# Performance work log

Measured on AMD Instinct MI355X. Metric: run time of the kernel, lower is better.

Reference implementation:

```python
import jax, jax.numpy as jnp
import numpy as np

N = 50000      # nodes in the block
M = 10         # mailbox_size
H = 8          # attention heads
DIN = 128      # dim_in (per-mail message dim)
DOUT = 128     # dim_out (memory dim)
DT = 128       # dim_time
LN_EPS = 1e-5
LRELU_SLOPE = 0.2


def setup_inputs() -> dict:
    key = jax.random.key(0)
    ks = jax.random.split(key, 16)
    s = 0.05  # small init scale for weights
    return {
        # forward tensor args
        "mem": jax.random.normal(ks[0], (N, DOUT), jnp.float32),
        "mem_input": jax.random.normal(ks[1], (N, M * DIN), jnp.float32),
        "ts": jax.random.uniform(ks[2], (N,), jnp.float32) * 100.0,
        "mail_ts": jax.random.uniform(ks[3], (N, M), jnp.float32) * 100.0,
        # learned parameters (torch Linear convention: W is [out, in])
        "wq_w": jax.random.normal(ks[4], (DOUT, DOUT), jnp.float32) * s,
        "wq_b": jnp.zeros((DOUT,), jnp.float32),
        "wk_w": jax.random.normal(ks[5], (DOUT, DIN + DT), jnp.float32) * s,
        "wk_b": jnp.zeros((DOUT,), jnp.float32),
        "wv_w": jax.random.normal(ks[6], (DOUT, DIN + DT), jnp.float32) * s,
        "wv_b": jnp.zeros((DOUT,), jnp.float32),
        "ln_g": jnp.ones((DOUT,), jnp.float32),
        "ln_b": jnp.zeros((DOUT,), jnp.float32),
        "mlp_w": jax.random.normal(ks[7], (DOUT, DOUT), jnp.float32) * s,
        "mlp_b": jnp.zeros((DOUT,), jnp.float32),
        # TimeEncode: cos(dt * te_w + te_b), te_w = 1/10^linspace(0,9,DT) as in TGN
        "te_w": (1.0 / (10.0 ** np.linspace(0, 9, DT))).astype(np.float32),
        "te_b": jnp.zeros((DT,), jnp.float32),
    }


def reference(mem, mem_input, ts, mail_ts,
              wq_w, wq_b, wk_w, wk_b, wv_w, wv_b,
              ln_g, ln_b, mlp_w, mlp_b, te_w, te_b):
    n = mem.shape[0]
    # Q: [n, H, Dh]
    Q = (mem @ wq_w.T + wq_b).reshape(n, H, -1)
    # mails: [n, M, DIN]
    mails = mem_input.reshape(n, M, -1)
    # time encoding of (src ts - mail ts): [n, M, DT]
    dt = ts[:, None] - mail_ts
    time_feat = jnp.cos(dt[:, :, None] * te_w + te_b)
    mails = jnp.concatenate([mails, time_feat], axis=2)  # [n, M, DIN+DT]
    K = (mails @ wk_w.T + wk_b).reshape(n, M, H, -1)
    V = (mails @ wv_w.T + wv_b).reshape(n, M, H, -1)
    # elementwise QK reduction over head dim, LeakyReLU, softmax over mailbox
    att = jnp.einsum('nhd,nmhd->nmh', Q, K)
    att = jax.nn.leaky_relu(att, LRELU_SLOPE)
    att = jax.nn.softmax(att, axis=1)          # (att_dropout = identity in eval)
    rst = jnp.einsum('nmh,nmhd->nhd', att, V).reshape(n, -1)
    rst = rst + mem                             # residual
    # LayerNorm
    mu = rst.mean(axis=-1, keepdims=True)
    var = ((rst - mu) ** 2).mean(axis=-1, keepdims=True)
    rst = (rst - mu) / jnp.sqrt(var + LN_EPS) * ln_g + ln_b
    # MLP + (dropout = identity in eval) + ReLU
    rst = rst @ mlp_w.T + mlp_b
    return jax.nn.relu(rst)
```

## Files before the change

### kernel.cpp

```cpp
#include <hip/hip_runtime.h>
#include <hip/hip_bf16.h>

#define N_NODES 50000
#define NB 32
#define NTILES 1563
#define PGRID 512
#define LN_EPS 1e-5f
#define SLOPE 0.2f

typedef __attribute__((ext_vector_type(8))) short bf16x8;
typedef __attribute__((ext_vector_type(4))) float f32x4;

__device__ __forceinline__ int imin(int a, int b){ return a < b ? a : b; }

__device__ __forceinline__ short f2bf(float f){
  union { float f; unsigned u; } v; v.f = f;
  unsigned r = v.u + 0x7fffu + ((v.u >> 16) & 1u);
  return (short)(r >> 16);
}

__device__ __forceinline__ float rsum16_dpp(float x){
  asm volatile(
    "s_nop 1\n\t"
    "v_add_f32_dpp %0, %0, %0 row_ror:8 row_mask:0xf bank_mask:0xf\n\t"
    "s_nop 1\n\t"
    "v_add_f32_dpp %0, %0, %0 row_ror:4 row_mask:0xf bank_mask:0xf\n\t"
    "s_nop 1\n\t"
    "v_add_f32_dpp %0, %0, %0 row_ror:2 row_mask:0xf bank_mask:0xf\n\t"
    "s_nop 1\n\t"
    "v_add_f32_dpp %0, %0, %0 row_ror:1 row_mask:0xf bank_mask:0xf"
    : "+v"(x));
  return x;
}

__device__ __forceinline__ unsigned cvtpk(float a, float b){
  unsigned r;
  asm("v_cvt_pk_bf16_f32 %0, %1, %2" : "=v"(r) : "v"(a), "v"(b));
  return r;
}

__device__ __forceinline__ bf16x8 pack8(float4 a, float4 b){
  union { unsigned u[4]; bf16x8 v; } r;
  r.u[0] = cvtpk(a.x, a.y); r.u[1] = cvtpk(a.z, a.w);
  r.u[2] = cvtpk(b.x, b.y); r.u[3] = cvtpk(b.z, b.w);
  return r.v;
}

#define WKP 0
#define WVP 32768
#define WQP 65536
#define MLPP 81920

__global__ __launch_bounds__(256) void prep_pack(
    const float* __restrict__ wq, const float* __restrict__ wk,
    const float* __restrict__ wv, const float* __restrict__ mlp,
    unsigned short* __restrict__ wsP)
{
  int idx = blockIdx.x * 256 + threadIdx.x;
  const float* src; int base, K, local;
  if (idx < 32768)      { src = wk;  base = WKP;  local = idx;         K = 256; }
  else if (idx < 65536) { src = wv;  base = WVP;  local = idx - 32768; K = 256; }
  else if (idx < 81920) { src = wq;  base = WQP;  local = idx - 65536; K = 128; }
  else if (idx < 98304) { src = mlp; base = MLPP; local = idx - 81920; K = 128; }
  else return;
  int i  = local & 7;
  int l  = (local >> 3) & 63;
  int nt = (local >> 9) & 7;
  int ks = local >> 12;
  int row = nt * 16 + (l & 15);
  int k   = ks * 32 + ((l >> 4) << 3) + i;
  wsP[base + local] = (unsigned short)f2bf(src[row * K + k]);
}

__device__ __forceinline__ void stage_write(
    unsigned short* sAp, const float* sTs, const float* sMts,
    const float* sTeW, const float* sTeB,
    float4 f0, float4 f1, int srow, int skc, int ssw, int sg, int m)
{
  float dt = sTs[srow] - sMts[srow*10 + m];
  const float4* tw = (const float4*)(sTeW + skc);
  const float4* tb = (const float4*)(sTeB + skc);
  float4 w0 = tw[0], w1 = tw[1];
  float4 b0 = tb[0], b1 = tb[1];
  float4 c0, c1;
  c0.x=__cosf(dt*w0.x+b0.x); c0.y=__cosf(dt*w0.y+b0.y); c0.z=__cosf(dt*w0.z+b0.z); c0.w=__cosf(dt*w0.w+b0.w);
  c1.x=__cosf(dt*w1.x+b1.x); c1.y=__cosf(dt*w1.y+b1.y); c1.z=__cosf(dt*w1.z+b1.z); c1.w=__cosf(dt*w1.w+b1.w);
  bf16x8* dst = (bf16x8*)sAp;
  dst[srow*32 + (sg ^ ssw)]      = pack8(f0, f1);
  dst[srow*32 + 16 + (sg ^ ssw)] = pack8(c0, c1);
}

__global__ __launch_bounds__(512, 2) void fused_tmu(
    const float* __restrict__ mem, const float* __restrict__ mem_input,
    const float* __restrict__ ts, const float* __restrict__ mail_ts,
    const float* __restrict__ wq_b, const float* __restrict__ wk_b,
    const float* __restrict__ wv_b, const float* __restrict__ ln_g,
    const float* __restrict__ ln_b, const float* __restrict__ mlp_b,
    const float* __restrict__ te_w, const float* __restrict__ te_b,
    const unsigned short* __restrict__ wsP, float* __restrict__ out)
{
  __shared__ __align__(16) unsigned short sA[2 * NB * 256];
  __shared__ float sTs[NB];
  __shared__ float sMts[NB * 10];
  __shared__ float sTeW[128], sTeB[128];
  __shared__ float sRed[NB * 16];

  const int tid  = threadIdx.x;
  const int lane = tid & 63;
  const int wid  = tid >> 6;
  const int l15  = lane & 15;
  const int lg   = lane >> 4;

  const int srow = tid >> 4;
  const int sg   = tid & 15;
  const int skc  = sg << 3;
  const int ssw  = srow & 7;

  if (tid < 128){ sTeW[tid] = te_w[tid]; sTeB[tid] = te_b[tid]; }

  const int c = wid * 16 + l15;
  float qb = wq_b[c], kb = wk_b[c], vb = wv_b[c];
  float lgv = ln_g[c], lbv = ln_b[c], mbv = mlp_b[c];

  const bf16x8* wsv = (const bf16x8*)wsP;
  bf16x8 wkf[8], wvf[8];
  #pragma unroll
  for (int ks = 0; ks < 8; ks++){
    wkf[ks] = wsv[WKP/8 + (ks*8 + wid)*64 + lane];
    wvf[ks] = wsv[WVP/8 + (ks*8 + wid)*64 + lane];
  }

  f32x4 z4 = {0.f, 0.f, 0.f, 0.f};

  for (int tb = blockIdx.x; tb < NTILES; tb += PGRID){
    const int node0 = tb * NB;
    const int sgn = imin(node0 + srow, N_NODES - 1);
    const float* miBase = mem_input + (size_t)sgn * 1280 + skc;

    float4 fm0, fm1, fa0, fa1;
    {
      const float4* mp = (const float4*)(mem + (size_t)sgn * 128 + skc);
      fm0 = mp[0]; fm1 = mp[1];
      const float4* mi0 = (const float4*)(miBase);
      fa0 = mi0[0]; fa1 = mi0[1];
    }
    if (tid < NB) sTs[tid] = ts[imin(node0 + tid, N_NODES - 1)];
    if (tid < NB * 10){
      int nn = tid / 10, mm = tid - nn * 10;
      sMts[tid] = mail_ts[(size_t)imin(node0 + nn, N_NODES - 1) * 10 + mm];
    }
    {
      bf16x8* dst = (bf16x8*)sA;
      dst[NB*32 + srow*32 + (sg ^ ssw)] = pack8(fm0, fm1);
    }
    bf16x8 wqf[4];
    #pragma unroll
    for (int ks = 0; ks < 4; ks++)
      wqf[ks] = wsv[WQP/8 + (ks*8 + wid)*64 + lane];

    __syncthreads();

    stage_write(sA, sTs, sMts, sTeW, sTeB, fa0, fa1, srow, skc, ssw, sg, 0);
    { const float4* mi1 = (const float4*)(miBase + 128); fa0 = mi1[0]; fa1 = mi1[1]; }

    f32x4 qac[2];
    qac[0] = (f32x4){qb, qb, qb, qb};
    qac[1] = qac[0];
    {
      const bf16x8* P1 = (const bf16x8*)sA + NB*32;
      #pragma unroll
      for (int ntr = 0; ntr < 2; ntr++){
        int r = ntr*16 + l15, rs = r & 7;
        #pragma unroll
        for (int ks = 0; ks < 4; ks++){
          bf16x8 af = P1[r*32 + ((ks*4 + lg) ^ rs)];
          qac[ntr] = __builtin_amdgcn_mfma_f32_16x16x32_bf16(af, wqf[ks], qac[ntr], 0, 0, 0);
        }
      }
    }

    __syncthreads();

    f32x4 pv[2] = {z4, z4};
    f32x4 sm[2] = {z4, z4};
    for (int m = 0; m < 10; m++){
      const bf16x8* P = (const bf16x8*)sA + (m & 1) * NB*32;
      #pragma unroll
      for (int ntr = 0; ntr < 2; ntr++){
        int r = ntr*16 + l15, rs = r & 7;
        f32x4 ka = z4, va = z4;
        #pragma unroll
        for (int ks = 0; ks < 8; ks++){
          bf16x8 af = P[r*32 + ((ks*4 + lg) ^ rs)];
          ka = __builtin_amdgcn_mfma_f32_16x16x32_bf16(af, wkf[ks], ka, 0, 0, 0);
          va = __builtin_amdgcn_mfma_f32_16x16x32_bf16(af, wvf[ks], va, 0, 0, 0);
        }
        #pragma unroll
        for (int j = 0; j < 4; j++){
          float lv = (ka[j] + kb) * qac[ntr][j];
          lv = rsum16_dpp(lv);
          lv = fmaxf(lv, SLOPE * lv);
          lv = fminf(lv, 60.f);
          float p = __expf(lv);
          sm[ntr][j] += p;
          pv[ntr][j] += p * va[j];
        }
      }
      if (m < 9){
        stage_write(sA + ((m+1) & 1) * NB*256, sTs, sMts, sTeW, sTeB,
                    fa0, fa1, srow, skc, ssw, sg, m+1);
        if (m < 8){
          const float4* mi = (const float4*)(miBase + (size_t)(m+2)*128);
          fa0 = mi[0]; fa1 = mi[1];
        }
      }
      __syncthreads();
    }

    float rstv[2][4];
    #pragma unroll
    for (int ntr = 0; ntr < 2; ntr++)
      #pragma unroll
      for (int j = 0; j < 4; j++){
        int gn = imin(node0 + ntr*16 + lg*4 + j, N_NODES - 1);
        rstv[ntr][j] = pv[ntr][j] / sm[ntr][j] + vb + mem[(size_t)gn * 128 + c];
      }
    #pragma unroll
    for (int ntr = 0; ntr < 2; ntr++)
      #pragma unroll
      for (int j = 0; j < 4; j++){
        float s = rsum16_dpp(rstv[ntr][j]);
        float q = rsum16_dpp(rstv[ntr][j] * rstv[ntr][j]);
        if (l15 == 0){
          int nl = ntr*16 + lg*4 + j;
          sRed[nl*16 + wid*2    ] = s;
          sRed[nl*16 + wid*2 + 1] = q;
        }
      }
    __syncthreads();
    #pragma unroll
    for (int ntr = 0; ntr < 2; ntr++)
      #pragma unroll
      for (int j = 0; j < 4; j++){
        int nl = ntr*16 + lg*4 + j;
        float sum = 0.f, sq = 0.f;
        #pragma unroll
        for (int w = 0; w < 8; w++){
          sum += sRed[nl*16 + w*2];
          sq  += sRed[nl*16 + w*2 + 1];
        }
        float mu  = sum * (1.f/128.f);
        float var = sq * (1.f/128.f) - mu*mu;
        float rs  = rsqrtf(var + LN_EPS);
        float y = (rstv[ntr][j] - mu) * rs * lgv + lbv;
        sA[nl*256 + ((c >> 3) ^ (nl & 7))*8 + (c & 7)] = (unsigned short)f2bf(y);
      }

    bf16x8 mlpf[4];
    #pragma unroll
    for (int ks = 0; ks < 4; ks++)
      mlpf[ks] = wsv[MLPP/8 + (ks*8 + wid)*64 + lane];
    __syncthreads();

    f32x4 mac[2];
    mac[0] = (f32x4){mbv, mbv, mbv, mbv};
    mac[1] = mac[0];
    {
      const bf16x8* P0 = (const bf16x8*)sA;
      #pragma unroll
      for (int ntr = 0; ntr < 2; ntr++){
        int r = ntr*16 + l15, rs = r & 7;
        #pragma unroll
        for (int ks = 0; ks < 4; ks++){
          bf16x8 af = P0[r*32 + ((ks*4 + lg) ^ rs)];
          mac[ntr] = __builtin_amdgcn_mfma_f32_16x16x32_bf16(af, mlpf[ks], mac[ntr], 0, 0, 0);
        }
      }
    }
    #pragma unroll
    for (int ntr = 0; ntr < 2; ntr++)
      #pragma unroll
      for (int j = 0; j < 4; j++){
        float o = fmaxf(mac[ntr][j], 0.f);
        int node = node0 + ntr*16 + lg*4 + j;
        if (node < N_NODES)
          out[(size_t)node * 128 + c] = o;
      }
  }
}

extern "C" void kernel_launch(void* const* d_in, const int* in_sizes, int n_in,
                              void* d_out, int out_size, void* d_ws, size_t ws_size,
                              hipStream_t stream)
{
  const float* mem       = (const float*)d_in[0];
  const float* mem_input = (const float*)d_in[1];
  const float* ts        = (const float*)d_in[2];
  const float* mail_ts   = (const float*)d_in[3];
  const float* wq_w      = (const float*)d_in[4];
  const float* wq_b      = (const float*)d_in[5];
  const float* wk_w      = (const float*)d_in[6];
  const float* wk_b      = (const float*)d_in[7];
  const float* wv_w      = (const float*)d_in[8];
  const float* wv_b      = (const float*)d_in[9];
  const float* ln_g      = (const float*)d_in[10];
  const float* ln_b      = (const float*)d_in[11];
  const float* mlp_w     = (const float*)d_in[12];
  const float* mlp_b     = (const float*)d_in[13];
  const float* te_w      = (const float*)d_in[14];
  const float* te_b      = (const float*)d_in[15];
  unsigned short* wsP = (unsigned short*)d_ws;
  float* outp = (float*)d_out;

  prep_pack<<<384, 256, 0, stream>>>(wq_w, wk_w, wv_w, mlp_w, wsP);
  fused_tmu<<<PGRID, 512, 0, stream>>>(mem, mem_input, ts, mail_ts,
      wq_b, wk_b, wv_b, ln_g, ln_b, mlp_b, te_w, te_b, wsP, outp);
}
```

Before: 135.3 us.

## Prefetch next tile's mem, timestamps and first mail into the previous iteration

```diff
diff --git a/kernel.cpp b/kernel.cpp
--- a/kernel.cpp
+++ b/kernel.cpp
@@ -132,16 +132,16 @@
 
   f32x4 z4 = {0.f, 0.f, 0.f, 0.f};
 
-  for (int tb = blockIdx.x; tb < NTILES; tb += PGRID){
+  int tb = blockIdx.x;
+  float4 fa0, fa1;
+  {
     const int node0 = tb * NB;
     const int sgn = imin(node0 + srow, N_NODES - 1);
-    const float* miBase = mem_input + (size_t)sgn * 1280 + skc;
-
-    float4 fm0, fm1, fa0, fa1;
+    float4 fm0, fm1;
     {
       const float4* mp = (const float4*)(mem + (size_t)sgn * 128 + skc);
       fm0 = mp[0]; fm1 = mp[1];
-      const float4* mi0 = (const float4*)(miBase);
+      const float4* mi0 = (const float4*)(mem_input + (size_t)sgn * 1280 + skc);
       fa0 = mi0[0]; fa1 = mi0[1];
     }
     if (tid < NB) sTs[tid] = ts[imin(node0 + tid, N_NODES - 1)];
@@ -149,20 +149,23 @@
       int nn = tid / 10, mm = tid - nn * 10;
       sMts[tid] = mail_ts[(size_t)imin(node0 + nn, N_NODES - 1) * 10 + mm];
     }
-    {
-      bf16x8* dst = (bf16x8*)sA;
-      dst[NB*32 + srow*32 + (sg ^ ssw)] = pack8(fm0, fm1);
-    }
+    bf16x8* dst = (bf16x8*)sA;
+    dst[NB*32 + srow*32 + (sg ^ ssw)] = pack8(fm0, fm1);
+  }
+  __syncthreads();
+
+  for (; tb < NTILES; tb += PGRID){
+    const int node0 = tb * NB;
+    const int sgn = imin(node0 + srow, N_NODES - 1);
+    const float* miBase = mem_input + (size_t)sgn * 1280 + skc;
+
+    stage_write(sA, sTs, sMts, sTeW, sTeB, fa0, fa1, srow, skc, ssw, sg, 0);
+    { const float4* mi1 = (const float4*)(miBase + 128); fa0 = mi1[0]; fa1 = mi1[1]; }
+
     bf16x8 wqf[4];
     #pragma unroll
     for (int ks = 0; ks < 4; ks++)
       wqf[ks] = wsv[WQP/8 + (ks*8 + wid)*64 + lane];
-
-    __syncthreads();
-
-    stage_write(sA, sTs, sMts, sTeW, sTeB, fa0, fa1, srow, skc, ssw, sg, 0);
-    { const float4* mi1 = (const float4*)(miBase + 128); fa0 = mi1[0]; fa1 = mi1[1]; }
-
     f32x4 qac[2];
     qac[0] = (f32x4){qb, qb, qb, qb};
     qac[1] = qac[0];
@@ -217,6 +220,11 @@
       __syncthreads();
     }
 
+    const int tn = tb + PGRID;
+    const bool has_next = tn < NTILES;
+    const int node0n = tn * NB;
+    const int sgnn = imin(node0n + srow, N_NODES - 1);
+
     float rstv[2][4];
     #pragma unroll
     for (int ntr = 0; ntr < 2; ntr++)
@@ -225,6 +233,13 @@
         int gn = imin(node0 + ntr*16 + lg*4 + j, N_NODES - 1);
         rstv[ntr][j] = pv[ntr][j] / sm[ntr][j] + vb + mem[(size_t)gn * 128 + c];
       }
+
+    float4 nf0, nf1;
+    if (has_next){
+      const float4* mp = (const float4*)(mem + (size_t)sgnn * 128 + skc);
+      nf0 = mp[0]; nf1 = mp[1];
+    }
+
     #pragma unroll
     for (int ntr = 0; ntr < 2; ntr++)
       #pragma unroll
@@ -238,6 +253,7 @@
         }
       }
     __syncthreads();
+
     #pragma unroll
     for (int ntr = 0; ntr < 2; ntr++)
       #pragma unroll
@@ -256,11 +272,26 @@
         sA[nl*256 + ((c >> 3) ^ (nl & 7))*8 + (c & 7)] = (unsigned short)f2bf(y);
       }
 
+    if (has_next){
+      if (tid < NB) sTs[tid] = ts[imin(node0n + tid, N_NODES - 1)];
+      if (tid < NB * 10){
+        int nn = tid / 10, mm = tid - nn * 10;
+        sMts[tid] = mail_ts[(size_t)imin(node0n + nn, N_NODES - 1) * 10 + mm];
+      }
+      bf16x8* dst = (bf16x8*)sA;
+      dst[NB*32 + srow*32 + (sg ^ ssw)] = pack8(nf0, nf1);
+    }
+
     bf16x8 mlpf[4];
     #pragma unroll
     for (int ks = 0; ks < 4; ks++)
       mlpf[ks] = wsv[MLPP/8 + (ks*8 + wid)*64 + lane];
     __syncthreads();
+
+    if (has_next){
+      const float4* mi0 = (const float4*)(mem_input + (size_t)sgnn * 1280 + skc);
+      fa0 = mi0[0]; fa1 = mi0[1];
+    }
 
     f32x4 mac[2];
     mac[0] = (f32x4){mbv, mbv, mbv, mbv};
@@ -286,6 +317,7 @@
         if (node < N_NODES)
           out[(size_t)node * 128 + c] = o;
       }
+    __syncthreads();
   }
 }
 
```

After: 135.2 us (median of 2 runs). No clear change (-0.1%).
